# Kernel tuning notes

Measured on AMD Instinct MI355X. Metric: run time of the kernel, lower is better.

## Reference

```python
import jax, jax.numpy as jnp
import numpy as np

E = 7          # ensemble_size
STATE = 32
ACTION = 8
HID = [256, 256, 256, 128]
B = 32768


def _init_linear(key, e, fan_in, fan_out):
    kw, kb = jax.random.split(key)
    bound = 1.0 / np.sqrt(fan_in)
    W = jax.random.uniform(kw, (e, fan_in, fan_out), jnp.float32, -bound, bound)
    b = jax.random.uniform(kb, (e, fan_out), jnp.float32, -bound, bound)
    return W, b


def setup_inputs() -> dict:
    key = jax.random.key(0)
    ks = jax.random.split(key, 9)
    state = jax.random.normal(ks[0], (B, STATE), jnp.float32)
    action = jax.random.normal(ks[1], (B, ACTION), jnp.float32)
    dims = [STATE + ACTION] + HID
    W0, b0 = _init_linear(ks[2], E, dims[0], dims[1])
    W1, b1 = _init_linear(ks[3], E, dims[1], dims[2])
    W2, b2 = _init_linear(ks[4], E, dims[2], dims[3])
    W3, b3 = _init_linear(ks[5], E, dims[3], dims[4])
    Wmu, bmu = _init_linear(ks[6], E, dims[4], STATE)
    Wsig, bsig = _init_linear(ks[7], E, dims[4], STATE)
    max_logstd = jnp.ones((STATE,), jnp.float32)
    min_logstd = jnp.full((STATE,), -5.0, jnp.float32)
    return {
        'state': state, 'action': action,
        'W0': W0, 'b0': b0, 'W1': W1, 'b1': b1,
        'W2': W2, 'b2': b2, 'W3': W3, 'b3': b3,
        'Wmu': Wmu, 'bmu': bmu, 'Wsig': Wsig, 'bsig': bsig,
        'max_logstd': max_logstd, 'min_logstd': min_logstd,
    }


def _swish(x):
    return x * jax.nn.sigmoid(x)


def _soft_clamp(x, _min, _max):
    x = _max - jax.nn.softplus(_max - x)
    x = _min + jax.nn.softplus(x - _min)
    return x


def reference(state, action, W0, b0, W1, b1, W2, b2, W3, b3,
              Wmu, bmu, Wsig, bsig, max_logstd, min_logstd):
    # Broadcast inputs to the ensemble axis: [E, B, D]
    x = jnp.concatenate([state, action], axis=-1)            # [B, S+A]
    h = jnp.broadcast_to(x, (E,) + x.shape)                   # [E, B, S+A]
    # Batched per-ensemble GEMM chain (grouped GEMM)
    h = _swish(jnp.einsum('ebi,eio->ebo', h, W0) + b0[:, None, :])
    h = _swish(jnp.einsum('ebi,eio->ebo', h, W1) + b1[:, None, :])
    h = _swish(jnp.einsum('ebi,eio->ebo', h, W2) + b2[:, None, :])
    h = _swish(jnp.einsum('ebi,eio->ebo', h, W3) + b3[:, None, :])
    mu = jnp.einsum('ebi,eio->ebo', h, Wmu) + bmu[:, None, :]         # [E, B, S]
    log_sigma = jnp.einsum('ebi,eio->ebo', h, Wsig) + bsig[:, None, :]
    log_sigma = _soft_clamp(log_sigma, min_logstd, max_logstd)
    sigma = jnp.exp(log_sigma)
    mu = mu + state[None, :, :]                                        # residual
    return mu, sigma
```

## Files before the change

kernel.cpp:

```cpp
#include <hip/hip_runtime.h>
#include <hip/hip_bf16.h>


#define NE 7
#define NB 32768
#define PER_E 188416
#define HSTRIDE 264

typedef __attribute__((ext_vector_type(8))) short short8;
typedef __attribute__((ext_vector_type(4))) float floatx4;

__device__ __forceinline__ short f2b(float f) {
    union { float f; unsigned u; } c; c.f = f;
    return (short)((c.u + 0x7fffu + ((c.u >> 16) & 1u)) >> 16);
}
__device__ __forceinline__ unsigned pk2(float a, float b) {
    union { __hip_bfloat162 h; unsigned u; } c;
    c.h = __float22bfloat162_rn(make_float2(a, b));
    return c.u;
}

__global__ void __launch_bounds__(256) pack_w(
    const float* __restrict__ W0, const float* __restrict__ W1,
    const float* __restrict__ W2, const float* __restrict__ W3,
    const float* __restrict__ Wmu, const float* __restrict__ Wsig,
    short* __restrict__ out)
{
    __shared__ float tile[32][65];
    const int t = threadIdx.x;
    int b = blockIdx.x;
    int e = b / 92;
    int r = b - e * 92;
    const float* src = W0;
    int off = 0, Kact = 40, N = 256, NT = 16, kt, ntb;
    bool inv = false, head = false;
    if (r < 8)       { kt = r >> 2; ntb = r & 3; }
    else if (r < 40) { r -= 8;  src = W1; off = 16384;  Kact = 256; kt = r >> 2; ntb = r & 3; inv = true; }
    else if (r < 72) { r -= 40; src = W2; off = 81920;  Kact = 256; kt = r >> 2; ntb = r & 3; inv = true; }
    else if (r < 88) { r -= 72; src = W3; off = 147456; Kact = 256; N = 128; NT = 8; kt = r >> 1; ntb = r & 1; inv = true; }
    else             { r -= 88; off = 180224; Kact = 128; N = 64; NT = 4; kt = r; ntb = 0; inv = true; head = true; }

#pragma unroll
    for (int i = 0; i < 8; ++i) {
        int elem  = t + i * 256;
        int row_l = elem >> 6, col_l = elem & 63;
        int gk = kt * 32 + row_l;
        int gn = ntb * 64 + col_l;
        float v = 0.f;
        if (gk < Kact) {
            if (head) v = (gn < 32) ? Wmu[((size_t)e * 128 + gk) * 32 + gn]
                                    : Wsig[((size_t)e * 128 + gk) * 32 + (gn - 32)];
            else      v = src[((size_t)e * Kact + gk) * N + gn];
        }
        tile[row_l][col_l] = v;
    }
    __syncthreads();

    const int f = t >> 6, lam = t & 63;
    const int lan = lam & 15, quad = lam >> 4;
    short8 o;
#pragma unroll
    for (int j = 0; j < 8; ++j) {
        int q  = quad * 8 + j;
        int sr = inv ? (((q & 1) << 4) | (q >> 1)) : q;
        o[j] = f2b(tile[sr][f * 16 + lan]);
    }
    *(short8*)(out + (size_t)e * PER_E + off +
               ((size_t)(kt * NT + ntb * 4 + f) * 64 + lam) * 8) = o;
}

template<int KT, int NTW, int NT, int NNTW>
__device__ __forceinline__ void mlp_layer(const short* __restrict__ wpk,
                                          const float* __restrict__ bias,
                                          short* hs, const int wave, const int lane,
                                          const short8* bf0,
                                          const short* __restrict__ nwpk,
                                          short8* nbf0) {
    const int quad = lane >> 4;
    const int lan  = lane & 15;
    floatx4 acc[4][NTW];
#pragma unroll
    for (int mt = 0; mt < 4; ++mt)
#pragma unroll
        for (int nt = 0; nt < NTW; ++nt) acc[mt][nt] = floatx4{0.f, 0.f, 0.f, 0.f};

    short8 bfc[NTW], bfn[NTW];
#pragma unroll
    for (int nt = 0; nt < NTW; ++nt) bfc[nt] = bf0[nt];

#pragma unroll
    for (int kt = 0; kt < KT; ++kt) {
        if (kt + 1 < KT) {
#pragma unroll
            for (int nt = 0; nt < NTW; ++nt)
                bfn[nt] = *(const short8*)(wpk +
                    ((size_t)((kt + 1) * NT + wave * NTW + nt) * 64 + lane) * 8);
        }
        short8 af[4];
#pragma unroll
        for (int mt = 0; mt < 4; ++mt)
            af[mt] = *(const short8*)(hs + (mt * 16 + lan) * HSTRIDE + kt * 32 + quad * 8);
#pragma unroll
        for (int nt = 0; nt < NTW; ++nt)
#pragma unroll
            for (int mt = 0; mt < 4; ++mt)
                acc[mt][nt] = __builtin_amdgcn_mfma_f32_16x16x32_bf16(af[mt], bfc[nt], acc[mt][nt], 0, 0, 0);
#pragma unroll
        for (int nt = 0; nt < NTW; ++nt) bfc[nt] = bfn[nt];
    }

#pragma unroll
    for (int nt = 0; nt < NNTW; ++nt)
        nbf0[nt] = *(const short8*)(nwpk + ((size_t)(wave * NNTW + nt) * 64 + lane) * 8);

    __syncthreads();
#pragma unroll
    for (int np = 0; np < NTW / 2; ++np) {
        const int ntg   = wave * NTW + 2 * np;
        const float bA  = bias[ntg * 16 + lan];
        const float bB  = bias[ntg * 16 + 16 + lan];
        const int pcol  = (ntg >> 1) * 32 + 2 * lan;
#pragma unroll
        for (int mt = 0; mt < 4; ++mt)
#pragma unroll
            for (int r2 = 0; r2 < 4; ++r2) {
                float vA = acc[mt][2 * np][r2] + bA;
                vA = vA * __builtin_amdgcn_rcpf(1.f + __expf(-vA));
                float vB = acc[mt][2 * np + 1][r2] + bB;
                vB = vB * __builtin_amdgcn_rcpf(1.f + __expf(-vB));
                *(unsigned*)(hs + (mt * 16 + quad * 4 + r2) * HSTRIDE + pcol) = pk2(vA, vB);
            }
    }
    __syncthreads();
}

__device__ __forceinline__ float softplus_stable(float x) {
    return fmaxf(x, 0.f) + __logf(1.f + __expf(-fabsf(x)));
}

__global__ void __launch_bounds__(256, 4)
fused_ensemble(const float* __restrict__ state, const float* __restrict__ action,
               const float* __restrict__ b0, const float* __restrict__ b1,
               const float* __restrict__ b2, const float* __restrict__ b3,
               const float* __restrict__ bmu, const float* __restrict__ bsig,
               const float* __restrict__ maxls, const float* __restrict__ minls,
               const short* __restrict__ wpk,
               float* __restrict__ out_mu, float* __restrict__ out_sig) {
    __shared__ __align__(16) short hs[64 * HSTRIDE];
    const int tid  = threadIdx.x;
    const int wave = tid >> 6, lane = tid & 63;
    const int bid  = blockIdx.x;
    const int e    = bid >> 9;
    const int r0   = (bid & 511) << 6;

    const short* wp = wpk + (size_t)e * PER_E;

    short8 fragA[4], fragB[4];
#pragma unroll
    for (int nt = 0; nt < 4; ++nt)
        fragA[nt] = *(const short8*)(wp + ((size_t)(wave * 4 + nt) * 64 + lane) * 8);

    for (int idx = tid; idx < 64 * 32; idx += 256) {
        int m = idx >> 5, cp = idx & 31;
        int row = r0 + m;
        float2 v;
        if (cp < 16)      v = ((const float2*)state)[row * 16 + cp];
        else if (cp < 20) v = ((const float2*)action)[row * 4 + (cp - 16)];
        else              v = make_float2(0.f, 0.f);
        *(unsigned*)(hs + m * HSTRIDE + 2 * cp) = pk2(v.x, v.y);
    }
    __syncthreads();

    mlp_layer<2, 4, 16, 4>(wp,          b0 + e * 256, hs, wave, lane, fragA, wp + 16384,  fragB);
    mlp_layer<8, 4, 16, 4>(wp + 16384,  b1 + e * 256, hs, wave, lane, fragB, wp + 81920,  fragA);
    mlp_layer<8, 4, 16, 2>(wp + 81920,  b2 + e * 256, hs, wave, lane, fragA, wp + 147456, fragB);
    mlp_layer<8, 2, 8, 1 >(wp + 147456, b3 + e * 128, hs, wave, lane, fragB, wp + 180224, fragA);

    const int quad = lane >> 4, lan = lane & 15;
    floatx4 acc[4];
#pragma unroll
    for (int mt = 0; mt < 4; ++mt) acc[mt] = floatx4{0.f, 0.f, 0.f, 0.f};
    const short* wph = wp + 180224;
    short8 bhc = fragA[0], bhn;
#pragma unroll
    for (int kt = 0; kt < 4; ++kt) {
        if (kt < 3)
            bhn = *(const short8*)(wph + (((size_t)(kt + 1) * 4 + wave) * 64 + lane) * 8);
#pragma unroll
        for (int mt = 0; mt < 4; ++mt) {
            const short8 af = *(const short8*)(hs + (mt * 16 + lan) * HSTRIDE + kt * 32 + quad * 8);
            acc[mt] = __builtin_amdgcn_mfma_f32_16x16x32_bf16(af, bhc, acc[mt], 0, 0, 0);
        }
        bhc = bhn;
    }
    const int colw = wave * 16 + lan;
    if (colw < 32) {
        const int col = colw;
        const float bv = bmu[e * 32 + col];
#pragma unroll
        for (int mt = 0; mt < 4; ++mt)
#pragma unroll
            for (int r2 = 0; r2 < 4; ++r2) {
                int grow = r0 + mt * 16 + quad * 4 + r2;
                float v = acc[mt][r2] + bv + state[grow * 32 + col];
                out_mu[((size_t)e * NB + grow) * 32 + col] = v;
            }
    } else {
        const int col = colw - 32;
        const float bv = bsig[e * 32 + col];
        const float mx = maxls[col], mn = minls[col];
#pragma unroll
        for (int mt = 0; mt < 4; ++mt)
#pragma unroll
            for (int r2 = 0; r2 < 4; ++r2) {
                int grow = r0 + mt * 16 + quad * 4 + r2;
                float ls = acc[mt][r2] + bv;
                ls = mx - softplus_stable(mx - ls);
                ls = mn + softplus_stable(ls - mn);
                out_sig[((size_t)e * NB + grow) * 32 + col] = __expf(ls);
            }
    }
}

extern "C" void kernel_launch(void* const* d_in, const int* in_sizes, int n_in,
                              void* d_out, int out_size, void* d_ws, size_t ws_size,
                              hipStream_t stream) {
    const float* state  = (const float*)d_in[0];
    const float* action = (const float*)d_in[1];
    const float* W0   = (const float*)d_in[2];
    const float* b0   = (const float*)d_in[3];
    const float* W1   = (const float*)d_in[4];
    const float* b1   = (const float*)d_in[5];
    const float* W2   = (const float*)d_in[6];
    const float* b2   = (const float*)d_in[7];
    const float* W3   = (const float*)d_in[8];
    const float* b3   = (const float*)d_in[9];
    const float* Wmu  = (const float*)d_in[10];
    const float* bmu  = (const float*)d_in[11];
    const float* Wsig = (const float*)d_in[12];
    const float* bsig = (const float*)d_in[13];
    const float* maxls = (const float*)d_in[14];
    const float* minls = (const float*)d_in[15];

    short* wpk = (short*)d_ws;
    float* out_mu  = (float*)d_out;
    float* out_sig = out_mu + (size_t)NE * NB * 32;

    pack_w<<<NE * 92, 256, 0, stream>>>(W0, W1, W2, W3, Wmu, Wsig, wpk);
    fused_ensemble<<<NE * 512, 256, 0, stream>>>(state, action, b0, b1, b2, b3,
                                                 bmu, bsig, maxls, minls, wpk,
                                                 out_mu, out_sig);
}
```

Measured before the change: 255.9 us.

## Use 8 waves per block, splitting N and M tiles across waves

Doubles the block to 512 threads. In the 256-wide layers each wave now owns 2 N-tiles instead of 4. In the 128-wide layer and the output head the work is split by M halves and N pairs, so each wave's per-layer MFMA work and register footprint shrink. The goal is more waves per CU to hide LDS and global latency during the GEMM chain. The cost is more barrier participants and duplicate A-fragment LDS reads across waves sharing the same rows.

```diff
diff --git a/kernel.cpp b/kernel.cpp
--- a/kernel.cpp
+++ b/kernel.cpp
@@ -69,18 +69,20 @@
                ((size_t)(kt * NT + ntb * 4 + f) * 64 + lam) * 8) = o;
 }
 
-template<int KT, int NTW, int NT, int NNTW>
+template<int KT, int NTW, int NT, int NNTW, int MTS>
 __device__ __forceinline__ void mlp_layer(const short* __restrict__ wpk,
                                           const float* __restrict__ bias,
-                                          short* hs, const int wave, const int lane,
+                                          short* hs, const int lane,
+                                          const int mtbase, const int ntbase,
                                           const short8* bf0,
                                           const short* __restrict__ nwpk,
+                                          const int nnbase,
                                           short8* nbf0) {
     const int quad = lane >> 4;
     const int lan  = lane & 15;
-    floatx4 acc[4][NTW];
-#pragma unroll
-    for (int mt = 0; mt < 4; ++mt)
+    floatx4 acc[MTS][NTW];
+#pragma unroll
+    for (int mt = 0; mt < MTS; ++mt)
 #pragma unroll
         for (int nt = 0; nt < NTW; ++nt) acc[mt][nt] = floatx4{0.f, 0.f, 0.f, 0.f};
 
@@ -94,16 +96,16 @@
 #pragma unroll
             for (int nt = 0; nt < NTW; ++nt)
                 bfn[nt] = *(const short8*)(wpk +
-                    ((size_t)((kt + 1) * NT + wave * NTW + nt) * 64 + lane) * 8);
+                    ((size_t)((kt + 1) * NT + ntbase + nt) * 64 + lane) * 8);
         }
-        short8 af[4];
-#pragma unroll
-        for (int mt = 0; mt < 4; ++mt)
-            af[mt] = *(const short8*)(hs + (mt * 16 + lan) * HSTRIDE + kt * 32 + quad * 8);
+        short8 af[MTS];
+#pragma unroll
+        for (int mt = 0; mt < MTS; ++mt)
+            af[mt] = *(const short8*)(hs + ((mtbase + mt) * 16 + lan) * HSTRIDE + kt * 32 + quad * 8);
 #pragma unroll
         for (int nt = 0; nt < NTW; ++nt)
 #pragma unroll
-            for (int mt = 0; mt < 4; ++mt)
+            for (int mt = 0; mt < MTS; ++mt)
                 acc[mt][nt] = __builtin_amdgcn_mfma_f32_16x16x32_bf16(af[mt], bfc[nt], acc[mt][nt], 0, 0, 0);
 #pragma unroll
         for (int nt = 0; nt < NTW; ++nt) bfc[nt] = bfn[nt];
@@ -111,24 +113,24 @@
 
 #pragma unroll
     for (int nt = 0; nt < NNTW; ++nt)
-        nbf0[nt] = *(const short8*)(nwpk + ((size_t)(wave * NNTW + nt) * 64 + lane) * 8);
+        nbf0[nt] = *(const short8*)(nwpk + ((size_t)(nnbase + nt) * 64 + lane) * 8);
 
     __syncthreads();
 #pragma unroll
     for (int np = 0; np < NTW / 2; ++np) {
-        const int ntg   = wave * NTW + 2 * np;
+        const int ntg   = ntbase + 2 * np;
         const float bA  = bias[ntg * 16 + lan];
         const float bB  = bias[ntg * 16 + 16 + lan];
         const int pcol  = (ntg >> 1) * 32 + 2 * lan;
 #pragma unroll
-        for (int mt = 0; mt < 4; ++mt)
+        for (int mt = 0; mt < MTS; ++mt)
 #pragma unroll
             for (int r2 = 0; r2 < 4; ++r2) {
                 float vA = acc[mt][2 * np][r2] + bA;
                 vA = vA * __builtin_amdgcn_rcpf(1.f + __expf(-vA));
                 float vB = acc[mt][2 * np + 1][r2] + bB;
                 vB = vB * __builtin_amdgcn_rcpf(1.f + __expf(-vB));
-                *(unsigned*)(hs + (mt * 16 + quad * 4 + r2) * HSTRIDE + pcol) = pk2(vA, vB);
+                *(unsigned*)(hs + ((mtbase + mt) * 16 + quad * 4 + r2) * HSTRIDE + pcol) = pk2(vA, vB);
             }
     }
     __syncthreads();
@@ -138,7 +140,7 @@
     return fmaxf(x, 0.f) + __logf(1.f + __expf(-fabsf(x)));
 }
 
-__global__ void __launch_bounds__(256, 4)
+__global__ void __launch_bounds__(512, 4)
 fused_ensemble(const float* __restrict__ state, const float* __restrict__ action,
                const float* __restrict__ b0, const float* __restrict__ b1,
                const float* __restrict__ b2, const float* __restrict__ b3,
@@ -155,12 +157,14 @@
 
     const short* wp = wpk + (size_t)e * PER_E;
 
-    short8 fragA[4], fragB[4];
-#pragma unroll
-    for (int nt = 0; nt < 4; ++nt)
-        fragA[nt] = *(const short8*)(wp + ((size_t)(wave * 4 + nt) * 64 + lane) * 8);
-
-    for (int idx = tid; idx < 64 * 32; idx += 256) {
+    const int npair = wave & 3, mhalf = wave >> 2;
+
+    short8 fragA[2], fragB[2];
+#pragma unroll
+    for (int nt = 0; nt < 2; ++nt)
+        fragA[nt] = *(const short8*)(wp + ((size_t)(wave * 2 + nt) * 64 + lane) * 8);
+
+    for (int idx = tid; idx < 64 * 32; idx += 512) {
         int m = idx >> 5, cp = idx & 31;
         int row = r0 + m;
         float2 v;
@@ -171,37 +175,37 @@
     }
     __syncthreads();
 
-    mlp_layer<2, 4, 16, 4>(wp,          b0 + e * 256, hs, wave, lane, fragA, wp + 16384,  fragB);
-    mlp_layer<8, 4, 16, 4>(wp + 16384,  b1 + e * 256, hs, wave, lane, fragB, wp + 81920,  fragA);
-    mlp_layer<8, 4, 16, 2>(wp + 81920,  b2 + e * 256, hs, wave, lane, fragA, wp + 147456, fragB);
-    mlp_layer<8, 2, 8, 1 >(wp + 147456, b3 + e * 128, hs, wave, lane, fragB, wp + 180224, fragA);
+    mlp_layer<2, 2, 16, 2, 4>(wp,          b0 + e * 256, hs, lane, 0, wave * 2, fragA, wp + 16384,  wave * 2,  fragB);
+    mlp_layer<8, 2, 16, 2, 4>(wp + 16384,  b1 + e * 256, hs, lane, 0, wave * 2, fragB, wp + 81920,  wave * 2,  fragA);
+    mlp_layer<8, 2, 16, 2, 4>(wp + 81920,  b2 + e * 256, hs, lane, 0, wave * 2, fragA, wp + 147456, npair * 2, fragB);
+    mlp_layer<8, 2, 8, 1, 2 >(wp + 147456, b3 + e * 128, hs, lane, mhalf * 2, npair * 2, fragB, wp + 180224, npair, fragA);
 
     const int quad = lane >> 4, lan = lane & 15;
-    floatx4 acc[4];
-#pragma unroll
-    for (int mt = 0; mt < 4; ++mt) acc[mt] = floatx4{0.f, 0.f, 0.f, 0.f};
+    floatx4 acc[2];
+#pragma unroll
+    for (int mt = 0; mt < 2; ++mt) acc[mt] = floatx4{0.f, 0.f, 0.f, 0.f};
     const short* wph = wp + 180224;
     short8 bhc = fragA[0], bhn;
 #pragma unroll
     for (int kt = 0; kt < 4; ++kt) {
         if (kt < 3)
-            bhn = *(const short8*)(wph + (((size_t)(kt + 1) * 4 + wave) * 64 + lane) * 8);
-#pragma unroll
-        for (int mt = 0; mt < 4; ++mt) {
-            const short8 af = *(const short8*)(hs + (mt * 16 + lan) * HSTRIDE + kt * 32 + quad * 8);
+            bhn = *(const short8*)(wph + (((size_t)(kt + 1) * 4 + npair) * 64 + lane) * 8);
+#pragma unroll
+        for (int mt = 0; mt < 2; ++mt) {
+            const short8 af = *(const short8*)(hs + ((mhalf * 2 + mt) * 16 + lan) * HSTRIDE + kt * 32 + quad * 8);
             acc[mt] = __builtin_amdgcn_mfma_f32_16x16x32_bf16(af, bhc, acc[mt], 0, 0, 0);
         }
         bhc = bhn;
     }
-    const int colw = wave * 16 + lan;
+    const int colw = npair * 16 + lan;
     if (colw < 32) {
         const int col = colw;
         const float bv = bmu[e * 32 + col];
 #pragma unroll
-        for (int mt = 0; mt < 4; ++mt)
+        for (int mt = 0; mt < 2; ++mt)
 #pragma unroll
             for (int r2 = 0; r2 < 4; ++r2) {
-                int grow = r0 + mt * 16 + quad * 4 + r2;
+                int grow = r0 + (mhalf * 2 + mt) * 16 + quad * 4 + r2;
                 float v = acc[mt][r2] + bv + state[grow * 32 + col];
                 out_mu[((size_t)e * NB + grow) * 32 + col] = v;
             }
@@ -210,10 +214,10 @@
         const float bv = bsig[e * 32 + col];
         const float mx = maxls[col], mn = minls[col];
 #pragma unroll
-        for (int mt = 0; mt < 4; ++mt)
+        for (int mt = 0; mt < 2; ++mt)
 #pragma unroll
             for (int r2 = 0; r2 < 4; ++r2) {
-                int grow = r0 + mt * 16 + quad * 4 + r2;
+                int grow = r0 + (mhalf * 2 + mt) * 16 + quad * 4 + r2;
                 float ls = acc[mt][r2] + bv;
                 ls = mx - softplus_stable(mx - ls);
                 ls = mn + softplus_stable(ls - mn);
@@ -247,7 +251,7 @@
     float* out_sig = out_mu + (size_t)NE * NB * 32;
 
     pack_w<<<NE * 92, 256, 0, stream>>>(W0, W1, W2, W3, Wmu, Wsig, wpk);
-    fused_ensemble<<<NE * 512, 256, 0, stream>>>(state, action, b0, b1, b2, b3,
+    fused_ensemble<<<NE * 512, 512, 0, stream>>>(state, action, b0, b1, b2, b3,
                                                  bmu, bsig, maxls, minls, wpk,
                                                  out_mu, out_sig);
 }
```

Result: faster. 231.5 us (-9.5%).
